# Performance work log

Measured on AMD Instinct MI355X. Metric: run time of the kernel, lower is better.

The kernel has to match this reference:

```python
import jax, jax.numpy as jnp
import numpy as np
from jax import lax

EPS_BN = 1e-5
EPS_NORM = 1e-12
D = 6                      # max_displacement
K = 2 * D + 1              # 13

def _conv(x, w, b, stride=1, pad=0):
    out = lax.conv_general_dilated(x, w, (stride, stride), [(pad, pad), (pad, pad)],
                                   dimension_numbers=('NCHW', 'OIHW', 'NCHW'))
    return out + b[None, :, None, None]

def _bn(x, g, be):
    m = x.mean(axis=(0, 2, 3), keepdims=True)
    v = x.var(axis=(0, 2, 3), keepdims=True)  # biased var, as torch BN uses for normalization
    return g[None, :, None, None] * (x - m) * lax.rsqrt(v + EPS_BN) + be[None, :, None, None]

def _lrelu(x):
    return jax.nn.leaky_relu(x, 0.1)

def _encoder(x, w1, b1, g1, be1, w2, b2, g2, be2, w3, b3, g3, be3):
    fine = _lrelu(_bn(_conv(x, w1, b1, pad=3), g1, be1))          # (B,16,64,64)
    h = _lrelu(_bn(_conv(fine, w2, b2, stride=2, pad=2), g2, be2))  # (B,32,32,32)
    coarse = _lrelu(_bn(_conv(h, w3, b3, pad=1), g3, be3))        # (B,32,32,32)
    return coarse, fine

def _l2norm_c(f):
    n = jnp.sqrt(jnp.sum(f * f, axis=1, keepdims=True))
    return f / jnp.maximum(n, EPS_NORM)

def _correlation(fA, fB):
    # cost[b, i*K+j, h, w] = sum_c fA_n[b,c,h,w] * fB_n_pad[b,c,h+i,w+j]
    B, C, H, W = fA.shape
    fA = _l2norm_c(fA)
    fB = _l2norm_c(fB)
    fBp = jnp.pad(fB, ((0, 0), (0, 0), (D, D), (D, D)))
    costs = []
    for i in range(K):          # small fixed displacement set (169 slices)
        for j in range(K):
            costs.append(jnp.sum(fA * fBp[:, :, i:i + H, j:j + W], axis=1))
    return jnp.stack(costs, axis=1)  # (B, K*K, H, W), matches unfold ordering

def _decoder(cost, skipA, skipB, wc1, bc1, wc2, bc2, wf1, bf1, wf2, bf2, wo, bo):
    x = _lrelu(_conv(cost, wc1, bc1, pad=1))
    x = _lrelu(_conv(x, wc2, bc2, pad=1))        # (B,64,32,32)
    x = jnp.repeat(jnp.repeat(x, 2, axis=2), 2, axis=3)
    x = jnp.concatenate([x, skipA, skipB], axis=1)       # (B,96,64,64)
    x = _lrelu(_conv(x, wf1, bf1, pad=1))
    x = _lrelu(_conv(x, wf2, bf2, pad=1))        # (B,32,64,64)
    return _conv(x, wo, bo, pad=0)               # (B,2,64,64)

def setup_inputs() -> dict:
    key = jax.random.key(0)
    ks = jax.random.split(key, 16)
    B = 32
    n_disp = K * K  # 169
    f32 = jnp.float32
    w = lambda k, shp: (jax.random.normal(k, shp, dtype=f32) * 0.05)
    inp = {
        'frameA': jax.random.normal(ks[0], (B, 1, 64, 64), dtype=f32),
        'frameB': jax.random.normal(ks[1], (B, 1, 64, 64), dtype=f32),
        # shared siamese encoder params
        'w1': w(ks[2], (16, 1, 7, 7)),  'b1': jnp.zeros((16,), f32),
        'g1': jnp.ones((16,), f32),     'be1': jnp.zeros((16,), f32),
        'w2': w(ks[3], (32, 16, 5, 5)), 'b2': jnp.zeros((32,), f32),
        'g2': jnp.ones((32,), f32),     'be2': jnp.zeros((32,), f32),
        'w3': w(ks[4], (32, 32, 3, 3)), 'b3': jnp.zeros((32,), f32),
        'g3': jnp.ones((32,), f32),     'be3': jnp.zeros((32,), f32),
        # decoder params
        'wc1': w(ks[5], (128, n_disp, 3, 3)), 'bc1': jnp.zeros((128,), f32),
        'wc2': w(ks[6], (64, 128, 3, 3)),     'bc2': jnp.zeros((64,), f32),
        'wf1': w(ks[7], (64, 96, 3, 3)),      'bf1': jnp.zeros((64,), f32),
        'wf2': w(ks[8], (32, 64, 3, 3)),      'bf2': jnp.zeros((32,), f32),
        'wo':  w(ks[9], (2, 32, 1, 1)),       'bo': jnp.zeros((2,), f32),
    }
    return inp

def reference(frameA, frameB, w1, b1, g1, be1, w2, b2, g2, be2, w3, b3, g3, be3,
              wc1, bc1, wc2, bc2, wf1, bf1, wf2, bf2, wo, bo):
    coarseA, skipA = _encoder(frameA, w1, b1, g1, be1, w2, b2, g2, be2, w3, b3, g3, be3)
    coarseB, skipB = _encoder(frameB, w1, b1, g1, be1, w2, b2, g2, be2, w3, b3, g3, be3)
    cost = _correlation(coarseA, coarseB)
    return _decoder(cost, skipA, skipB, wc1, bc1, wc2, bc2, wf1, bf1, wf2, bf2, wo, bo)
```

## Files before the change

kernel.cpp:

```cpp
#include <hip/hip_runtime.h>

typedef __attribute__((ext_vector_type(4))) float f32x4;
typedef __attribute__((ext_vector_type(8))) short bf16x8;

#define BN_EPS 1e-5f
constexpr int BATCH = 32;

static inline int cdiv(int a, int b) { return (a + b - 1) / b; }

__device__ __forceinline__ float lrelu(float v) { return v > 0.f ? v : 0.1f * v; }

__device__ __forceinline__ unsigned short f2bf(float f) {
    unsigned u = __float_as_uint(f);
    u = (u + 0x7FFFu + ((u >> 16) & 1u)) >> 16;
    return (unsigned short)u;
}
__device__ __forceinline__ float bf2f(unsigned short s) {
    return __uint_as_float(((unsigned)s) << 16);
}

#define SWZ(e)  ((e) ^ ((((e) >> 6) & 3) << 3))
#define FSWZ(e) ((e) ^ ((((e) >> 5) & 7) << 2))
#define CSWZ(c, w) ((c) ^ (((w) & 7) << 2))

template<int C, int NS>
__device__ __forceinline__ void finalize_stats(const float2* __restrict__ part, int f,
                                               float inv, float* sstats)
{
    __shared__ float2 red[256];
    int t = threadIdx.x;
    int c = t % C, k = t / C;
    float s1 = 0.f, s2 = 0.f;
    for (int q = k; q < NS; q += 256 / C) {
        float2 p = part[(size_t)(f * C + c) * NS + q];
        s1 += p.x; s2 += p.y;
    }
    red[t] = make_float2(s1, s2);
    __syncthreads();
    for (int off = 128; off >= C; off >>= 1) {
        if (t < off) { red[t].x += red[t + off].x; red[t].y += red[t + off].y; }
        __syncthreads();
    }
    if (t < C) {
        float m = red[t].x * inv;
        float var = red[t].y * inv - m * m;
        sstats[2 * t]     = m;
        sstats[2 * t + 1] = rsqrtf(var + BN_EPS);
    }
    __syncthreads();
}

__global__ __launch_bounds__(256) void conv1_prep(
    const float* __restrict__ fA, const float* __restrict__ fB,
    const float* __restrict__ w, const float* __restrict__ bias,
    unsigned short* __restrict__ outN, float2* __restrict__ part1,
    const float* wd1, const float* wd2, const float* wd3, const float* wd4,
    const float* wE2s, const float* wE3s,
    unsigned short* d1, unsigned short* d2, unsigned short* d3,
    unsigned short* d4, unsigned short* dE2, unsigned short* dE3)
{
    const int gid = blockIdx.x;
    if (gid >= 512) {
        int idx = (gid - 512) * 256 + threadIdx.x;
        if (idx < 368640) {
            const float* src; unsigned short* dst; int COUT, CINS, CINP;
            if (idx < 221184)      { src = wd1; dst = d1; COUT = 128; CINS = 169; CINP = 192; }
            else if (idx < 294912) { src = wd2; dst = d2; COUT = 64;  CINS = 128; CINP = 128; idx -= 221184; }
            else if (idx < 350208) { src = wd3; dst = d3; COUT = 64;  CINS = 96;  CINP = 96;  idx -= 294912; }
            else                   { src = wd4; dst = d4; COUT = 32;  CINS = 64;  CINP = 64;  idx -= 350208; }
            int ic  = idx % CINP;
            int oc  = (idx / CINP) % COUT;
            int tap = idx / (CINP * COUT);
            float v = (ic < CINS) ? src[((size_t)oc * CINS + ic) * 9 + tap] : 0.f;
            dst[((size_t)tap * COUT + oc) * CINP + ic] = f2bf(v);
        } else if (idx < 381952) {
            idx -= 368640;
            int c = idx % 32, oc = (idx / 32) % 32, s = idx / 1024;
            int tap = 2 * s + (c >= 16 ? 1 : 0);
            int ic = c & 15;
            float v = (tap < 25) ? wE2s[((size_t)oc * 16 + ic) * 25 + tap] : 0.f;
            dE2[idx] = f2bf(v);
        } else if (idx < 391168) {
            idx -= 381952;
            int ic = idx % 32, oc = (idx / 32) % 32, tap = idx / 1024;
            dE3[idx] = f2bf(wE3s[((size_t)oc * 32 + ic) * 9 + tap]);
        }
        return;
    }

    __shared__ float s_in[38][40];
    __shared__ float s_w[49][8];
    __shared__ float2 red1[4][8];

    const int tid = threadIdx.x;
    const int tx = tid & 15, ty = tid >> 4;
    const int tile = gid & 3;
    const int ocbase = ((gid >> 2) & 1) * 8;
    const int n = gid >> 3;
    const int x0 = (tile & 1) << 5;
    const int y0 = (tile >> 1) << 5;
    const float* in = (n < BATCH) ? (fA + (size_t)n * 4096) : (fB + (size_t)(n - BATCH) * 4096);

    for (int t = tid; t < 49 * 8; t += 256) {
        int oc = t & 7, k = t >> 3;
        s_w[k][oc] = w[(ocbase + oc) * 49 + k];
    }
    for (int t = tid; t < 38 * 38; t += 256) {
        int y = t / 38, x = t - (t / 38) * 38;
        int gy = y0 + y - 3, gx = x0 + x - 3;
        float v = 0.f;
        if ((unsigned)gy < 64u && (unsigned)gx < 64u) v = in[gy * 64 + gx];
        s_in[y][x] = v;
    }
    __syncthreads();

    float acc[8][4];
    #pragma unroll
    for (int oc = 0; oc < 8; ++oc) {
        float bv = bias[ocbase + oc];
        acc[oc][0] = bv; acc[oc][1] = bv; acc[oc][2] = bv; acc[oc][3] = bv;
    }
    #pragma unroll
    for (int kh = 0; kh < 7; ++kh) {
        #pragma unroll
        for (int kw = 0; kw < 7; ++kw) {
            float i00 = s_in[ty + kh][tx + kw];
            float i01 = s_in[ty + kh][tx + 16 + kw];
            float i10 = s_in[ty + 16 + kh][tx + kw];
            float i11 = s_in[ty + 16 + kh][tx + 16 + kw];
            #pragma unroll
            for (int oc = 0; oc < 8; ++oc) {
                float wv = s_w[kh * 7 + kw][oc];
                acc[oc][0] = fmaf(i00, wv, acc[oc][0]);
                acc[oc][1] = fmaf(i01, wv, acc[oc][1]);
                acc[oc][2] = fmaf(i10, wv, acc[oc][2]);
                acc[oc][3] = fmaf(i11, wv, acc[oc][3]);
            }
        }
    }
    #pragma unroll
    for (int i = 0; i < 2; ++i)
        #pragma unroll
        for (int j = 0; j < 2; ++j) {
            int k = i * 2 + j;
            int oy = y0 + ty + i * 16, ox = x0 + tx + j * 16;
            ushort4 p0, p1;
            p0.x = f2bf(acc[0][k]); p0.y = f2bf(acc[1][k]);
            p0.z = f2bf(acc[2][k]); p0.w = f2bf(acc[3][k]);
            p1.x = f2bf(acc[4][k]); p1.y = f2bf(acc[5][k]);
            p1.z = f2bf(acc[6][k]); p1.w = f2bf(acc[7][k]);
            unsigned short* dst = outN + ((size_t)n * 4096 + oy * 64 + ox) * 16 + ocbase;
            *(ushort4*)dst = p0;
            *(ushort4*)(dst + 4) = p1;
        }
    float v1[8], v2[8];
    #pragma unroll
    for (int oc = 0; oc < 8; ++oc) {
        v1[oc] = acc[oc][0] + acc[oc][1] + acc[oc][2] + acc[oc][3];
        v2[oc] = acc[oc][0] * acc[oc][0] + acc[oc][1] * acc[oc][1]
               + acc[oc][2] * acc[oc][2] + acc[oc][3] * acc[oc][3];
    }
    #pragma unroll
    for (int off = 32; off > 0; off >>= 1)
        #pragma unroll
        for (int oc = 0; oc < 8; ++oc) {
            v1[oc] += __shfl_down(v1[oc], off);
            v2[oc] += __shfl_down(v2[oc], off);
        }
    int wid = tid >> 6, lane = tid & 63;
    if (lane == 0)
        #pragma unroll
        for (int oc = 0; oc < 8; ++oc) red1[wid][oc] = make_float2(v1[oc], v2[oc]);
    __syncthreads();
    if (tid < 8) {
        float2 s = red1[0][tid];
        #pragma unroll
        for (int q = 1; q < 4; ++q) { s.x += red1[q][tid].x; s.y += red1[q][tid].y; }
        int f = n >> 5, slot = tile * 32 + (n & 31);
        part1[(size_t)(f * 16 + ocbase + tid) * 128 + slot] = s;
    }
}

template<int CIN, int COUT, int H, int TH, int MODE, int OM, int INBN>
__global__ __launch_bounds__(256) void conv3x3_mfma(
    const unsigned short* __restrict__ in,
    const unsigned short* __restrict__ in2,
    const unsigned short* __restrict__ wT,
    const float* __restrict__ bias,
    unsigned short* __restrict__ out,
    float* __restrict__ dout,
    const float* __restrict__ w1x1,
    const float* __restrict__ b1x1,
    const float2* __restrict__ partIn,
    const float* __restrict__ gIn,
    const float* __restrict__ beIn,
    float2* __restrict__ partOut)
{
    constexpr int MB = (COUT >= 64) ? 64 : COUT;
    constexpr int MFRAGS = MB / 16;
    constexpr int WM = 2;
    constexpr int MW = MFRAGS / WM;
    constexpr int NW = 4 / MW;
    constexpr int WN = TH / NW;

    __shared__ unsigned short s_w[9 * MB * 32];
    __shared__ unsigned short s_in[(TH + 2) * 18 * 32];
    __shared__ float sstIn[64];

    const int tid  = threadIdx.x;
    const int wid  = tid >> 6;
    const int lane = tid & 63;
    const int l15  = lane & 15;
    const int kg   = lane >> 4;
    constexpr int TILESX = H / 16;
    const int bx = blockIdx.x;
    const int x0 = (bx % TILESX) * 16;
    const int y0 = (bx / TILESX) * TH;
    const int ocbase = blockIdx.y * MB;
    const int n = blockIdx.z;

    const int mw = wid % MW;
    const int nw = wid / MW;

    if constexpr (INBN == 1)
        finalize_stats<32, 128>(partIn, 0, 1.f / (32.f * 4096.f), sstIn);
    if constexpr (INBN == 2)
        finalize_stats<32, 256>(partIn, n >> 5, 1.f / (32.f * 1024.f), sstIn);

    f32x4 acc[WM][WN];
    #pragma unroll
    for (int i = 0; i < WM; ++i) {
        #pragma unroll
        for (int r = 0; r < 4; ++r) {
            float bv = bias[ocbase + (mw * WM + i) * 16 + kg * 4 + r];
            #pragma unroll
            for (int j = 0; j < WN; ++j) acc[i][j][r] = bv;
        }
    }

    for (int c0 = 0; c0 < CIN; c0 += 32) {
        for (int t = tid; t < 9 * MB * 4; t += 256) {
            int sub = t & 3;
            int row = t >> 2;
            int tap = row / MB, oc = row % MB;
            const unsigned short* src = wT + ((size_t)(tap * COUT + ocbase + oc) * CIN + c0) + sub * 8;
            *(int4*)&s_w[SWZ(row * 32 + sub * 8)] = *(const int4*)src;
        }
        for (int t = tid; t < (TH + 2) * 18 * 4; t += 256) {
            int sub = t & 3;
            int p = t >> 2;
            int y = p / 18, x = p - y * 18;
            int gy = y0 - 1 + y, gx = x0 - 1 + x;
            int4 v = {0, 0, 0, 0};
            if ((unsigned)gy < (unsigned)H && (unsigned)gx < (unsigned)H) {
                if (MODE == 0) {
                    v = *(const int4*)&in[((size_t)(n * H + gy) * H + gx) * CIN + c0 + sub * 8];
                    if constexpr (INBN == 2) {
                        unsigned short* e = (unsigned short*)&v;
                        #pragma unroll
                        for (int k = 0; k < 8; ++k) {
                            int c = c0 + sub * 8 + k;
                            float xv = bf2f(e[k]);
                            e[k] = f2bf(lrelu((xv - sstIn[2 * c]) * sstIn[2 * c + 1] * gIn[c] + beIn[c]));
                        }
                    }
                } else {
                    if (c0 < 64) {
                        v = *(const int4*)&in[((size_t)(n * 32 + (gy >> 1)) * 32 + (gx >> 1)) * 64 + c0 + sub * 8];
                    } else {
                        int f  = sub >> 1;
                        int cc = (sub & 1) * 8;
                        v = *(const int4*)&in2[((size_t)((f * BATCH + n) * 64 + gy) * 64 + gx) * 16 + cc];
                        if constexpr (INBN == 1) {
                            unsigned short* e = (unsigned short*)&v;
                            #pragma unroll
                            for (int k = 0; k < 8; ++k) {
                                int gch = f * 16 + cc + k;
                                float xv = bf2f(e[k]);
                                e[k] = f2bf(lrelu((xv - sstIn[2 * gch]) * sstIn[2 * gch + 1]
                                                  * gIn[cc + k] + beIn[cc + k]));
                            }
                        }
                    }
                }
            }
            *(int4*)&s_in[SWZ(p * 32 + sub * 8)] = v;
        }
        __syncthreads();

        #pragma unroll
        for (int tap = 0; tap < 9; ++tap) {
            const int kh = tap / 3, kw = tap - (tap / 3) * 3;
            bf16x8 a[WM], b[WN];
            #pragma unroll
            for (int i = 0; i < WM; ++i) {
                int mf = mw * WM + i;
                a[i] = *(const bf16x8*)&s_w[SWZ((tap * MB + mf * 16 + l15) * 32 + kg * 8)];
            }
            #pragma unroll
            for (int j = 0; j < WN; ++j) {
                int nf = nw * WN + j;
                b[j] = *(const bf16x8*)&s_in[SWZ(((nf + kh) * 18 + l15 + kw) * 32 + kg * 8)];
            }
            #pragma unroll
            for (int i = 0; i < WM; ++i)
                #pragma unroll
                for (int j = 0; j < WN; ++j)
                    acc[i][j] = __builtin_amdgcn_mfma_f32_16x16x32_bf16(a[i], b[j], acc[i][j], 0, 0, 0);
        }
        __syncthreads();
    }

    if constexpr (OM == 2) {
        __shared__ unsigned short sC[16 * 16 * 32];
        #pragma unroll
        for (int i = 0; i < WM; ++i) {
            #pragma unroll
            for (int j = 0; j < WN; ++j) {
                int pos = (nw * WN + j) * 16 + l15;
                int e = pos * 32 + (mw * WM + i) * 16 + kg * 4;
                ushort4 pk;
                pk.x = f2bf(lrelu(acc[i][j][0]));
                pk.y = f2bf(lrelu(acc[i][j][1]));
                pk.z = f2bf(lrelu(acc[i][j][2]));
                pk.w = f2bf(lrelu(acc[i][j][3]));
                *(ushort4*)&sC[FSWZ(e)] = pk;
            }
        }
        __syncthreads();
        float a0 = b1x1[0], a1 = b1x1[1];
        #pragma unroll
        for (int q = 0; q < 8; ++q) {
            int e = tid * 32 + q * 4;
            ushort4 v = *(const ushort4*)&sC[FSWZ(e)];
            int c = q * 4;
            float x0v = bf2f(v.x), x1v = bf2f(v.y), x2v = bf2f(v.z), x3v = bf2f(v.w);
            a0 = fmaf(x0v, w1x1[c], a0);     a1 = fmaf(x0v, w1x1[32 + c], a1);
            a0 = fmaf(x1v, w1x1[c + 1], a0); a1 = fmaf(x1v, w1x1[32 + c + 1], a1);
            a0 = fmaf(x2v, w1x1[c + 2], a0); a1 = fmaf(x2v, w1x1[32 + c + 2], a1);
            a0 = fmaf(x3v, w1x1[c + 3], a0); a1 = fmaf(x3v, w1x1[32 + c + 3], a1);
        }
        int row = tid >> 4, col = tid & 15;
        int gy = y0 + row, gx = x0 + col;
        dout[((size_t)n * 2) * 4096 + gy * 64 + gx]     = a0;
        dout[((size_t)n * 2 + 1) * 4096 + gy * 64 + gx] = a1;
    } else {
        #pragma unroll
        for (int i = 0; i < WM; ++i) {
            int oc = ocbase + (mw * WM + i) * 16 + kg * 4;
            #pragma unroll
            for (int j = 0; j < WN; ++j) {
                int nf = nw * WN + j;
                int gy = y0 + nf, gx = x0 + l15;
                size_t base = ((size_t)(n * H + gy) * H + gx) * COUT + oc;
                if (OM == 0) {
                    ushort4 pk;
                    pk.x = f2bf(lrelu(acc[i][j][0]));
                    pk.y = f2bf(lrelu(acc[i][j][1]));
                    pk.z = f2bf(lrelu(acc[i][j][2]));
                    pk.w = f2bf(lrelu(acc[i][j][3]));
                    *(ushort4*)&out[base] = pk;
                } else {
                    *(f32x4*)&((float*)out)[base] = acc[i][j];
                }
            }
        }
    }

    if constexpr (OM == 3) {
        __shared__ float2 redC[4][4][8];
        float t1[2][4], t2[2][4];
        #pragma unroll
        for (int i = 0; i < 2; ++i)
            #pragma unroll
            for (int r = 0; r < 4; ++r) {
                float v0 = acc[i][0][r], v1 = acc[i][1][r];
                t1[i][r] = v0 + v1;
                t2[i][r] = v0 * v0 + v1 * v1;
            }
        #pragma unroll
        for (int off = 8; off > 0; off >>= 1)
            #pragma unroll
            for (int i = 0; i < 2; ++i)
                #pragma unroll
                for (int r = 0; r < 4; ++r) {
                    t1[i][r] += __shfl_down(t1[i][r], off);
                    t2[i][r] += __shfl_down(t2[i][r], off);
                }
        if (l15 == 0) {
            #pragma unroll
            for (int i = 0; i < 2; ++i)
                #pragma unroll
                for (int r = 0; r < 4; ++r)
                    redC[nw][kg][i * 4 + r] = make_float2(t1[i][r], t2[i][r]);
        }
        __syncthreads();
        if (tid < 32) {
            int oc = tid;
            int i = oc >> 4, kq = (oc & 15) >> 2, r = oc & 3;
            float2 s = redC[0][kq][i * 4 + r];
            #pragma unroll
            for (int q = 1; q < 4; ++q) {
                float2 p = redC[q][kq][i * 4 + r];
                s.x += p.x; s.y += p.y;
            }
            int f = n >> 5, slot = bx * 32 + (n & 31);
            partOut[(size_t)(f * 32 + oc) * 256 + slot] = s;
        }
    }
}

__global__ __launch_bounds__(256) void conv2s_mfma(
    const unsigned short* __restrict__ in, const unsigned short* __restrict__ wS,
    const float* __restrict__ bias, unsigned short* __restrict__ outN,
    const float2* __restrict__ part1, const float* __restrict__ g1,
    const float* __restrict__ be1, float2* __restrict__ part2)
{
    __shared__ unsigned short s_w[13 * 32 * 32];
    __shared__ unsigned short s_in[20 * 36 * 16];
    __shared__ float2 redC[4][4][8];
    __shared__ float sst[32];

    const int tid = threadIdx.x;
    const int nw  = tid >> 6;
    const int lane = tid & 63;
    const int l15 = lane & 15;
    const int kg  = lane >> 4;
    const int x0 = (blockIdx.x & 1) * 16;
    const int y0 = (blockIdx.x >> 1) * 8;
    const int n  = blockIdx.z;

    finalize_stats<16, 128>(part1, n >> 5, 1.f / (32.f * 4096.f), sst);

    f32x4 acc[2][2];
    #pragma unroll
    for (int i = 0; i < 2; ++i) {
        #pragma unroll
        for (int r = 0; r < 4; ++r) {
            float bv = bias[i * 16 + kg * 4 + r];
            acc[i][0][r] = bv; acc[i][1][r] = bv;
        }
    }

    for (int t = tid; t < 1664; t += 256) {
        int sub = t & 3, row = t >> 2;
        *(int4*)&s_w[SWZ(row * 32 + sub * 8)] = *(const int4*)&wS[row * 32 + sub * 8];
    }
    for (int t = tid; t < 1440; t += 256) {
        int sub = t & 1, p = t >> 1;
        int y = p / 36, x = p - y * 36;
        int gy = 2 * y0 - 2 + y, gx = 2 * x0 - 2 + x;
        int4 v = {0, 0, 0, 0};
        if ((unsigned)gy < 64u && (unsigned)gx < 64u) {
            v = *(const int4*)&in[((size_t)(n * 64 + gy) * 64 + gx) * 16 + sub * 8];
            unsigned short* e = (unsigned short*)&v;
            #pragma unroll
            for (int k = 0; k < 8; ++k) {
                int c = sub * 8 + k;
                float xv = bf2f(e[k]);
                e[k] = f2bf(lrelu((xv - sst[2 * c]) * sst[2 * c + 1] * g1[c] + be1[c]));
            }
        }
        *(int4*)&s_in[SWZ((y * 36 + x) * 16 + sub * 8)] = v;
    }
    __syncthreads();

    #pragma unroll
    for (int s = 0; s < 13; ++s) {
        int tA = 2 * s, tB = 2 * s + 1;
        int khA = tA / 5, kwA = tA % 5;
        int khB = tB / 5, kwB = tB % 5;
        int kh = (kg < 2) ? khA : khB;
        int kw = (kg < 2) ? kwA : kwB;
        int co = (kg & 1) * 8;
        bf16x8 a[2], b[2];
        a[0] = *(const bf16x8*)&s_w[SWZ((s * 32 + l15) * 32 + kg * 8)];
        a[1] = *(const bf16x8*)&s_w[SWZ((s * 32 + 16 + l15) * 32 + kg * 8)];
        #pragma unroll
        for (int j = 0; j < 2; ++j) {
            int py = nw * 2 + j;
            b[j] = *(const bf16x8*)&s_in[SWZ(((2 * py + kh) * 36 + 2 * l15 + kw) * 16 + co)];
        }
        acc[0][0] = __builtin_amdgcn_mfma_f32_16x16x32_bf16(a[0], b[0], acc[0][0], 0, 0, 0);
        acc[0][1] = __builtin_amdgcn_mfma_f32_16x16x32_bf16(a[0], b[1], acc[0][1], 0, 0, 0);
        acc[1][0] = __builtin_amdgcn_mfma_f32_16x16x32_bf16(a[1], b[0], acc[1][0], 0, 0, 0);
        acc[1][1] = __builtin_amdgcn_mfma_f32_16x16x32_bf16(a[1], b[1], acc[1][1], 0, 0, 0);
    }

    #pragma unroll
    for (int i = 0; i < 2; ++i)
        #pragma unroll
        for (int j = 0; j < 2; ++j) {
            int gy = y0 + nw * 2 + j, gx = x0 + l15;
            ushort4 pk;
            pk.x = f2bf(acc[i][j][0]); pk.y = f2bf(acc[i][j][1]);
            pk.z = f2bf(acc[i][j][2]); pk.w = f2bf(acc[i][j][3]);
            *(ushort4*)&outN[((size_t)(n * 32 + gy) * 32 + gx) * 32 + i * 16 + kg * 4] = pk;
        }

    float t1[2][4], t2[2][4];
    #pragma unroll
    for (int i = 0; i < 2; ++i)
        #pragma unroll
        for (int r = 0; r < 4; ++r) {
            float v0 = acc[i][0][r], v1 = acc[i][1][r];
            t1[i][r] = v0 + v1;
            t2[i][r] = v0 * v0 + v1 * v1;
        }
    #pragma unroll
    for (int off = 8; off > 0; off >>= 1)
        #pragma unroll
        for (int i = 0; i < 2; ++i)
            #pragma unroll
            for (int r = 0; r < 4; ++r) {
                t1[i][r] += __shfl_down(t1[i][r], off);
                t2[i][r] += __shfl_down(t2[i][r], off);
            }
    if (l15 == 0) {
        #pragma unroll
        for (int i = 0; i < 2; ++i)
            #pragma unroll
            for (int r = 0; r < 4; ++r)
                redC[nw][kg][i * 4 + r] = make_float2(t1[i][r], t2[i][r]);
    }
    __syncthreads();
    if (tid < 32) {
        int oc = tid;
        int i = oc >> 4, kq = (oc & 15) >> 2, r = oc & 3;
        float2 s = redC[0][kq][i * 4 + r];
        #pragma unroll
        for (int q = 1; q < 4; ++q) {
            float2 p = redC[q][kq][i * 4 + r];
            s.x += p.x; s.y += p.y;
        }
        int f = n >> 5, slot = blockIdx.x * 32 + (n & 31);
        part2[(size_t)(f * 32 + oc) * 256 + slot] = s;
    }
}

__global__ __launch_bounds__(256) void bn3_l2n_nhwc(const float* __restrict__ xN,
                             const float2* __restrict__ part3,
                             const float* __restrict__ g, const float* __restrict__ be,
                             float* __restrict__ outN)
{
    __shared__ float sst[64];
    int idx = blockIdx.x * blockDim.x + threadIdx.x;
    int f = idx >> 15;
    finalize_stats<32, 256>(part3, f, 1.f / (32.f * 1024.f), sst);
    const float* src = xN + (size_t)idx * 32;
    float v[32];
    float ss = 0.f;
    #pragma unroll
    for (int c = 0; c < 32; ++c) {
        float t = lrelu((src[c] - sst[2 * c]) * sst[2 * c + 1] * g[c] + be[c]);
        v[c] = t; ss += t * t;
    }
    float inv = 1.f / fmaxf(sqrtf(ss), 1e-12f);
    float* dst = outN + (size_t)idx * 32;
    #pragma unroll
    for (int c = 0; c < 32; ++c) dst[c] = v[c] * inv;
}

__global__ __launch_bounds__(256) void corr_split(const float* __restrict__ xN,
                                                  unsigned short* __restrict__ cost)
{
    __shared__ float sA[32 * 32];
    __shared__ float sB[7][32 * 32];
    __shared__ unsigned short sC[32][96];

    const int h = blockIdx.x, b = blockIdx.y, half = blockIdx.z;
    const int ROWS = half ? 6 : 7;
    const float* Ab = xN + ((size_t)b * 1024 + h * 32) * 32;
    const float* Bb = xN + ((size_t)(BATCH + b) * 1024) * 32;

    {
        int t = threadIdx.x;
        int w = t >> 3, gr = t & 7;
        f32x4 v = *(const f32x4*)&Ab[w * 32 + gr * 4];
        *(f32x4*)&sA[w * 32 + CSWZ(gr * 4, w)] = v;
    }
    for (int t = threadIdx.x; t < ROWS * 256; t += 256) {
        int row = t >> 8, q = t & 255;
        int w = q >> 3, gr = q & 7;
        int gh = h + half * 7 + row - 6;
        f32x4 v = {0.f, 0.f, 0.f, 0.f};
        if ((unsigned)gh < 32u) v = *(const f32x4*)&Bb[((size_t)gh * 32 + w) * 32 + gr * 4];
        *(f32x4*)&sB[row][w * 32 + CSWZ(gr * 4, w)] = v;
    }
    __syncthreads();

    const int w = threadIdx.x & 31;
    const int gq = threadIdx.x >> 5;
    if (gq < ROWS) {
        f32x4 a[8];
        #pragma unroll
        for (int gr = 0; gr < 8; ++gr) a[gr] = *(const f32x4*)&sA[w * 32 + CSWZ(gr * 4, w)];
        #pragma unroll
        for (int dx = 0; dx < 13; ++dx) {
            int wb = w + dx - 6;
            float s = 0.f;
            if ((unsigned)wb < 32u) {
                #pragma unroll
                for (int gr = 0; gr < 8; ++gr) {
                    f32x4 bv = *(const f32x4*)&sB[gq][wb * 32 + CSWZ(gr * 4, wb)];
                    s += a[gr].x * bv.x + a[gr].y * bv.y + a[gr].z * bv.z + a[gr].w * bv.w;
                }
            }
            sC[w][gq * 13 + dx] = f2bf(s);
        }
    }
    __syncthreads();

    const int ND = ROWS * 13;
    for (int t = threadIdx.x; t < 32 * ND; t += 256) {
        int ww = t / ND;
        int d  = t - ww * ND;
        cost[((size_t)(b * 1024) + h * 32 + ww) * 192 + half * 91 + d] = sC[ww][d];
    }
}

extern "C" void kernel_launch(void* const* d_in, const int* in_sizes, int n_in,
                              void* d_out, int out_size, void* d_ws, size_t ws_size,
                              hipStream_t stream)
{
    const float* frameA = (const float*)d_in[0];
    const float* frameB = (const float*)d_in[1];
    const float* w1  = (const float*)d_in[2];
    const float* b1  = (const float*)d_in[3];
    const float* g1  = (const float*)d_in[4];
    const float* be1 = (const float*)d_in[5];
    const float* w2  = (const float*)d_in[6];
    const float* b2  = (const float*)d_in[7];
    const float* g2  = (const float*)d_in[8];
    const float* be2 = (const float*)d_in[9];
    const float* w3  = (const float*)d_in[10];
    const float* b3  = (const float*)d_in[11];
    const float* g3  = (const float*)d_in[12];
    const float* be3 = (const float*)d_in[13];
    const float* wc1 = (const float*)d_in[14];
    const float* bc1 = (const float*)d_in[15];
    const float* wc2 = (const float*)d_in[16];
    const float* bc2 = (const float*)d_in[17];
    const float* wf1 = (const float*)d_in[18];
    const float* bf1 = (const float*)d_in[19];
    const float* wf2 = (const float*)d_in[20];
    const float* bf2 = (const float*)d_in[21];
    const float* wo  = (const float*)d_in[22];
    const float* bo  = (const float*)d_in[23];

    float* ws      = (float*)d_ws;
    float* c3N     = ws;
    float* coarseN = c3N + 2097152;
    float2* part1  = (float2*)(coarseN + 2097152);
    float2* part2  = part1 + 4096;
    float2* part3  = part2 + 16384;
    unsigned short* fineN = (unsigned short*)(part3 + 16384);
    unsigned short* h2bf  = fineN + 4194304;
    unsigned short* costN = h2bf + 2097152;
    unsigned short* d1    = costN + 6291456;
    unsigned short* d2    = d1 + 4194304;
    unsigned short* f1o   = d2 + 2097152;
    unsigned short* wT1   = f1o + 8388608;
    unsigned short* wT2   = wT1 + 221184;
    unsigned short* wTf1  = wT2 + 73728;
    unsigned short* wTf2  = wTf1 + 55296;
    unsigned short* wE2   = wTf2 + 18432;
    unsigned short* wE3   = wE2 + 13312;

    const int T = 256;

    conv1_prep<<<2040, T, 0, stream>>>(frameA, frameB, w1, b1, fineN, part1,
                                       wc1, wc2, wf1, wf2, w2, w3,
                                       wT1, wT2, wTf1, wTf2, wE2, wE3);

    conv2s_mfma<<<dim3(8, 1, 64), T, 0, stream>>>(fineN, wE2, b2, h2bf,
                                                  part1, g1, be1, part2);

    conv3x3_mfma<32, 32, 32, 8, 0, 3, 2><<<dim3(8, 1, 64), T, 0, stream>>>(
        h2bf, nullptr, wE3, b3, (unsigned short*)c3N, nullptr, nullptr, nullptr,
        part2, g2, be2, part3);

    bn3_l2n_nhwc<<<256, T, 0, stream>>>(c3N, part3, g3, be3, coarseN);

    corr_split<<<dim3(32, BATCH, 2), T, 0, stream>>>(coarseN, costN);

    conv3x3_mfma<192, 128, 32, 8, 0, 0, 0><<<dim3(8, 2, BATCH), T, 0, stream>>>(
        costN, nullptr, wT1, bc1, d1, nullptr, nullptr, nullptr,
        nullptr, nullptr, nullptr, nullptr);
    conv3x3_mfma<128, 64, 32, 8, 0, 0, 0><<<dim3(8, 1, BATCH), T, 0, stream>>>(
        d1, nullptr, wT2, bc2, d2, nullptr, nullptr, nullptr,
        nullptr, nullptr, nullptr, nullptr);
    conv3x3_mfma<96, 64, 64, 8, 1, 0, 1><<<dim3(32, 1, BATCH), T, 0, stream>>>(
        d2, fineN, wTf1, bf1, f1o, nullptr, nullptr, nullptr,
        part1, g1, be1, nullptr);
    conv3x3_mfma<64, 32, 64, 16, 0, 2, 0><<<dim3(16, 1, BATCH), T, 0, stream>>>(
        f1o, nullptr, wTf2, bf2, nullptr, (float*)d_out, wo, bo,
        nullptr, nullptr, nullptr, nullptr);
}
```

Measured before the change: 195.7 us.

## Pre-swizzle weights into LDS image layout and load via global_load_lds

The weight-prep kernel now writes the bf16 conv weights already permuted into the exact swizzled LDS image for each input-channel chunk and output-channel block. The conv kernels can then copy those images straight into shared memory with the global-to-LDS DMA builtin, instead of computing per-thread indices and doing register-staged swizzled stores. The goal is to cut VGPR traffic and address arithmetic in the weight staging loop, and to let the encoder conv overlap its weight load with the stats finalization. The risk is correctness: it relies on the global_load_lds builtin with 16-byte width and on the host-side layout matching the kernel-side chunk indexing exactly.

```diff
diff --git a/kernel.cpp b/kernel.cpp
--- a/kernel.cpp
+++ b/kernel.cpp
@@ -22,6 +22,14 @@
 #define SWZ(e)  ((e) ^ ((((e) >> 6) & 3) << 3))
 #define FSWZ(e) ((e) ^ ((((e) >> 5) & 7) << 2))
 #define CSWZ(c, w) ((c) ^ (((w) & 7) << 2))
+
+__device__ __forceinline__ void gload16(const unsigned short* g, unsigned short* l)
+{
+    __builtin_amdgcn_global_load_lds(
+        (const __attribute__((address_space(1))) void*)g,
+        (__attribute__((address_space(3))) void*)l,
+        16, 0, 0);
+}
 
 template<int C, int NS>
 __device__ __forceinline__ void finalize_stats(const float2* __restrict__ part, int f,
@@ -63,27 +71,41 @@
     if (gid >= 512) {
         int idx = (gid - 512) * 256 + threadIdx.x;
         if (idx < 368640) {
-            const float* src; unsigned short* dst; int COUT, CINS, CINP;
-            if (idx < 221184)      { src = wd1; dst = d1; COUT = 128; CINS = 169; CINP = 192; }
-            else if (idx < 294912) { src = wd2; dst = d2; COUT = 64;  CINS = 128; CINP = 128; idx -= 221184; }
-            else if (idx < 350208) { src = wd3; dst = d3; COUT = 64;  CINS = 96;  CINP = 96;  idx -= 294912; }
-            else                   { src = wd4; dst = d4; COUT = 32;  CINS = 64;  CINP = 64;  idx -= 350208; }
-            int ic  = idx % CINP;
-            int oc  = (idx / CINP) % COUT;
-            int tap = idx / (CINP * COUT);
+            const float* src; unsigned short* dst; int MB, NOCB, CINS, COUT;
+            if (idx < 221184)      { src = wd1; dst = d1; MB = 64; NOCB = 2; CINS = 169; COUT = 128; }
+            else if (idx < 294912) { src = wd2; dst = d2; MB = 64; NOCB = 1; CINS = 128; COUT = 64; idx -= 221184; }
+            else if (idx < 350208) { src = wd3; dst = d3; MB = 64; NOCB = 1; CINS = 96;  COUT = 64; idx -= 294912; }
+            else                   { src = wd4; dst = d4; MB = 32; NOCB = 1; CINS = 64;  COUT = 32; idx -= 350208; }
+            int lid = idx;
+            int IMG = 9 * MB * 32;
+            int chunk = lid / (NOCB * IMG);
+            int r = lid % (NOCB * IMG);
+            int ocb = r / IMG;
+            int y = r % IMG;
+            int z = SWZ(y);
+            int row = z >> 5;
+            int tap = (MB == 64) ? (row >> 6) : (row >> 5);
+            int oc  = ocb * MB + (row & (MB - 1));
+            int ic  = chunk * 32 + (z & 31);
             float v = (ic < CINS) ? src[((size_t)oc * CINS + ic) * 9 + tap] : 0.f;
-            dst[((size_t)tap * COUT + oc) * CINP + ic] = f2bf(v);
+            dst[lid] = f2bf(v);
         } else if (idx < 381952) {
-            idx -= 368640;
-            int c = idx % 32, oc = (idx / 32) % 32, s = idx / 1024;
-            int tap = 2 * s + (c >= 16 ? 1 : 0);
+            int lid = idx - 368640;
+            int z = SWZ(lid);
+            int row = z >> 5;
+            int slot = row >> 5, ocr = row & 31;
+            int c = z & 31;
+            int tap = 2 * slot + (c >= 16 ? 1 : 0);
             int ic = c & 15;
-            float v = (tap < 25) ? wE2s[((size_t)oc * 16 + ic) * 25 + tap] : 0.f;
-            dE2[idx] = f2bf(v);
+            float v = (tap < 25) ? wE2s[((size_t)ocr * 16 + ic) * 25 + tap] : 0.f;
+            dE2[lid] = f2bf(v);
         } else if (idx < 391168) {
-            idx -= 381952;
-            int ic = idx % 32, oc = (idx / 32) % 32, tap = idx / 1024;
-            dE3[idx] = f2bf(wE3s[((size_t)oc * 32 + ic) * 9 + tap]);
+            int lid = idx - 381952;
+            int z = SWZ(lid);
+            int row = z >> 5;
+            int tap = row >> 5, ocr = row & 31;
+            int ic = z & 31;
+            dE3[lid] = f2bf(wE3s[((size_t)ocr * 32 + ic) * 9 + tap]);
         }
         return;
     }
@@ -202,8 +224,11 @@
     constexpr int MW = MFRAGS / WM;
     constexpr int NW = 4 / MW;
     constexpr int WN = TH / NW;
-
-    __shared__ unsigned short s_w[9 * MB * 32];
+    constexpr int NOCB = COUT / MB;
+    constexpr int WIMG = 9 * MB * 32;
+    constexpr int WTOT = WIMG / 512;
+
+    __shared__ unsigned short s_w[WIMG];
     __shared__ unsigned short s_in[(TH + 2) * 18 * 32];
     __shared__ float sstIn[64];
 
@@ -239,12 +264,10 @@
     }
 
     for (int c0 = 0; c0 < CIN; c0 += 32) {
-        for (int t = tid; t < 9 * MB * 4; t += 256) {
-            int sub = t & 3;
-            int row = t >> 2;
-            int tap = row / MB, oc = row % MB;
-            const unsigned short* src = wT + ((size_t)(tap * COUT + ocbase + oc) * CIN + c0) + sub * 8;
-            *(int4*)&s_w[SWZ(row * 32 + sub * 8)] = *(const int4*)src;
+        {
+            const unsigned short* wsrc = wT + ((size_t)((c0 >> 5) * NOCB + blockIdx.y)) * WIMG;
+            for (int i = wid; i < WTOT; i += 4)
+                gload16(wsrc + i * 512 + lane * 8, &s_w[i * 512]);
         }
         for (int t = tid; t < (TH + 2) * 18 * 4; t += 256) {
             int sub = t & 3;
@@ -430,6 +453,9 @@
     const int y0 = (blockIdx.x >> 1) * 8;
     const int n  = blockIdx.z;
 
+    for (int i = nw; i < 26; i += 4)
+        gload16(wS + i * 512 + lane * 8, &s_w[i * 512]);
+
     finalize_stats<16, 128>(part1, n >> 5, 1.f / (32.f * 4096.f), sst);
 
     f32x4 acc[2][2];
@@ -442,10 +468,6 @@
         }
     }
 
-    for (int t = tid; t < 1664; t += 256) {
-        int sub = t & 3, row = t >> 2;
-        *(int4*)&s_w[SWZ(row * 32 + sub * 8)] = *(const int4*)&wS[row * 32 + sub * 8];
-    }
     for (int t = tid; t < 1440; t += 256) {
         int sub = t & 1, p = t >> 1;
         int y = p / 36, x = p - y * 36;
```

Result: faster. 171.0 us (-12.6%).
